# Performance work log

Hardware: AMD Instinct MI355X
Metric: run time of the kernel (lower is better)

The kernel has to match this reference:

```python
import jax, jax.numpy as jnp
import numpy as np

D_MODEL = 1024
D_FF = 4096
NUM_EXPERTS = 8
TOP_K = 2


def setup_inputs() -> dict:
    key = jax.random.key(0)
    ks = jax.random.split(key, 9)
    s = 0.02
    x = jax.random.normal(ks[0], (2, 2048, D_MODEL), dtype=jnp.float32)
    Wg = jax.random.normal(ks[1], (D_MODEL, NUM_EXPERTS), dtype=jnp.float32) * s
    bg = jnp.zeros((NUM_EXPERTS,), dtype=jnp.float32)
    W1 = jax.random.normal(ks[2], (NUM_EXPERTS, D_MODEL, D_FF), dtype=jnp.float32) * s
    b1 = jnp.zeros((NUM_EXPERTS, D_FF), dtype=jnp.float32)
    W3 = jax.random.normal(ks[3], (NUM_EXPERTS, D_MODEL, D_FF), dtype=jnp.float32) * s
    b3 = jnp.zeros((NUM_EXPERTS, D_FF), dtype=jnp.float32)
    W2 = jax.random.normal(ks[4], (NUM_EXPERTS, D_FF, D_MODEL), dtype=jnp.float32) * s
    b2 = jnp.zeros((NUM_EXPERTS, D_MODEL), dtype=jnp.float32)
    return {"x": x, "Wg": Wg, "bg": bg, "W1": W1, "b1": b1,
            "W3": W3, "b3": b3, "W2": W2, "b2": b2}


def reference(x, Wg, bg, W1, b1, W3, b3, W2, b2):
    # Gate (eval mode: no gaussian noise, no dropout)
    logits = x @ Wg + bg                                  # [b, s, E]
    probs = jax.nn.softmax(logits, axis=-1)
    top_v, top_i = jax.lax.top_k(probs, TOP_K)            # [b, s, K]
    top_v = top_v / (top_v.sum(axis=-1, keepdims=True) + 1e-6)
    # combine[b,s,e] = sum_k top_v[b,s,k] * 1[top_i[b,s,k]==e]
    onehot = jax.nn.one_hot(top_i, NUM_EXPERTS, dtype=x.dtype)  # [b, s, K, E]
    combine = jnp.einsum('bsk,bske->bse', top_v, onehot)        # [b, s, E]

    out = jnp.zeros_like(x)
    for e in range(NUM_EXPERTS):
        # SwiGLU expert FFN applied densely; masked-out tokens zeroed by combine weight
        h = jax.nn.silu(x @ W1[e] + b1[e]) * (x @ W3[e] + b3[e])   # [b, s, d_ff]
        out = out + combine[..., e:e + 1] * (h @ W2[e] + b2[e])
    return out
```

## Files before the change

kernel.cpp:

```cpp
#include <hip/hip_runtime.h>
#include <stdint.h>

#define D_MODEL 1024
#define D_FF    4096
#define NE      8
#define T_TOK   4096
#define R_TOT   8192

typedef float f32x4 __attribute__((ext_vector_type(4)));
typedef __bf16 bf16x8 __attribute__((ext_vector_type(8)));
typedef unsigned short ushort_t;

__device__ __forceinline__ ushort_t f2bf(float f) {
    unsigned int u = __float_as_uint(f);
    u += 0x7FFFu + ((u >> 16) & 1u);
    return (ushort_t)(u >> 16);
}

__device__ __forceinline__ void async16(const void* g, const void* l) {
    __builtin_amdgcn_global_load_lds(
        (const __attribute__((address_space(1))) unsigned int*)(uintptr_t)g,
        (__attribute__((address_space(3))) unsigned int*)(uintptr_t)l,
        16, 0, 0);
}

__global__ __launch_bounds__(256) void k_gate(
    const float* __restrict__ x, const float* __restrict__ Wg, const float* __restrict__ bg,
    int* __restrict__ topi, float* __restrict__ topw, int* __restrict__ counts)
{
    int wave = threadIdx.x >> 6, lane = threadIdx.x & 63;
    int t = blockIdx.x * 4 + wave;
    const float* xr = x + (size_t)t * D_MODEL;
    float acc[NE];
#pragma unroll
    for (int e = 0; e < NE; ++e) acc[e] = 0.f;
#pragma unroll
    for (int i = 0; i < D_MODEL / 64; ++i) {
        int k = i * 64 + lane;
        float xv = xr[k];
        const float4* wgp = (const float4*)(Wg + (size_t)k * NE);
        float4 w0 = wgp[0], w1 = wgp[1];
        acc[0] += xv * w0.x; acc[1] += xv * w0.y; acc[2] += xv * w0.z; acc[3] += xv * w0.w;
        acc[4] += xv * w1.x; acc[5] += xv * w1.y; acc[6] += xv * w1.z; acc[7] += xv * w1.w;
    }
#pragma unroll
    for (int off = 32; off >= 1; off >>= 1)
#pragma unroll
        for (int e = 0; e < NE; ++e) acc[e] += __shfl_down(acc[e], off, 64);
    if (lane == 0) {
        float l[NE], m = -1e30f;
#pragma unroll
        for (int e = 0; e < NE; ++e) { l[e] = acc[e] + bg[e]; m = fmaxf(m, l[e]); }
        float p[NE], Z = 0.f;
#pragma unroll
        for (int e = 0; e < NE; ++e) { p[e] = __expf(l[e] - m); Z += p[e]; }
        float invZ = 1.f / Z;
        int i0 = 0; float v0 = -1.f;
#pragma unroll
        for (int e = 0; e < NE; ++e) { p[e] *= invZ; if (p[e] > v0) { v0 = p[e]; i0 = e; } }
        int i1 = 0; float v1 = -1.f;
#pragma unroll
        for (int e = 0; e < NE; ++e) { if (e != i0 && p[e] > v1) { v1 = p[e]; i1 = e; } }
        float denom = 1.f / (v0 + v1 + 1e-6f);
        topi[t * 2 + 0] = i0; topi[t * 2 + 1] = i1;
        topw[t * 2 + 0] = v0 * denom; topw[t * 2 + 1] = v1 * denom;
        atomicAdd(&counts[i0], 1); atomicAdd(&counts[i1], 1);
    }
}

__global__ void k_scan(const int* __restrict__ counts, int* __restrict__ offsets,
                       int* __restrict__ cursors)
{
    if (threadIdx.x == 0) {
        int acc = 0;
        for (int e = 0; e < NE; ++e) { offsets[e] = acc; cursors[e] = acc; acc += counts[e]; }
    }
}

__global__ __launch_bounds__(256) void k_scatter(
    const int* __restrict__ topi_in, const float* __restrict__ topw,
    int* __restrict__ cursors, int* __restrict__ btok, float* __restrict__ bw)
{
    int t = blockIdx.x * 256 + threadIdx.x;
    int* topi = (int*)topi_in;
#pragma unroll
    for (int k = 0; k < 2; ++k) {
        int e = topi[t * 2 + k];
        int p = atomicAdd(&cursors[e], 1);
        btok[p] = t;
        bw[p] = topw[t * 2 + k];
        topi[t * 2 + k] = p;
    }
}

__global__ __launch_bounds__(256) void k_gather(
    const float* __restrict__ x, const int* __restrict__ btok, ushort_t* __restrict__ Xg)
{
    int i = blockIdx.x;
    int t = btok[i];
    float4 v = ((const float4*)(x + (size_t)t * D_MODEL))[threadIdx.x];
    ushort4 o;
    o.x = f2bf(v.x); o.y = f2bf(v.y); o.z = f2bf(v.z); o.w = f2bf(v.w);
    ((ushort4*)(Xg + (size_t)i * D_MODEL))[threadIdx.x] = o;
}

__global__ __launch_bounds__(256) void k_transpose(
    const float* __restrict__ W, ushort_t* __restrict__ Wt, int K, int N)
{
    __shared__ ushort_t tile[64 * 76];
    int e = blockIdx.z;
    const float* We = W + (size_t)e * K * N;
    ushort_t* Wte = Wt + (size_t)e * K * N;
    int nb = blockIdx.x * 64, kb = blockIdx.y * 64;
    int tn4 = (threadIdx.x & 15) * 4;
    int tk = threadIdx.x >> 4;
#pragma unroll
    for (int r = 0; r < 4; ++r) {
        int k = r * 16 + tk;
        float4 v = *(const float4*)(We + (size_t)(kb + k) * N + nb + tn4);
        tile[(tn4 + 0) * 76 + k] = f2bf(v.x);
        tile[(tn4 + 1) * 76 + k] = f2bf(v.y);
        tile[(tn4 + 2) * 76 + k] = f2bf(v.z);
        tile[(tn4 + 3) * 76 + k] = f2bf(v.w);
    }
    __syncthreads();
#pragma unroll
    for (int c = 0; c < 4; ++c) {
        int chunk = c * 256 + threadIdx.x;
        int n = chunk >> 4, kc = (chunk & 15) * 4;
        ushort4 o = *(const ushort4*)&tile[n * 76 + kc];
        *(ushort4*)(Wte + (size_t)(nb + n) * K + kb + kc) = o;
    }
}


__global__ __launch_bounds__(256, 2) void k_gemm1(
    const ushort_t* __restrict__ Xg, const ushort_t* __restrict__ W1t,
    const ushort_t* __restrict__ W3t,
    const float* __restrict__ b1, const float* __restrict__ b3,
    const int* __restrict__ counts, const int* __restrict__ offsets,
    ushort_t* __restrict__ H)
{
    __shared__ __align__(16) ushort_t sA [2][128 * 32];
    __shared__ __align__(16) ushort_t sB1[2][128 * 32];
    __shared__ __align__(16) ushort_t sB3[2][128 * 32];

    int bx = blockIdx.x;
    int lx = (bx & 7) * 9 + (bx >> 3);

    int tm = lx, e = 0, cnt = 0;
    for (; e < NE; ++e) {
        cnt = counts[e];
        int nt = (cnt + 127) >> 7;
        if (tm < nt) break;
        tm -= nt;
    }
    if (e >= NE) return;
    int row0 = offsets[e] + tm * 128;
    int rows_left = cnt - tm * 128;

    int tile_n = blockIdx.y * 128;
    int tid = threadIdx.x, wave = tid >> 6, lane = tid & 63;
    int wm = (wave >> 1) * 64, wn = (wave & 1) * 64;
    int col = lane & 15, quad = lane >> 4;

    const ushort_t* W1e = W1t + (size_t)e * D_FF * D_MODEL;
    const ushort_t* W3e = W3t + (size_t)e * D_FF * D_MODEL;

    const ushort_t* gA[2]; const ushort_t* gB1[2]; const ushort_t* gB3[2];
    unsigned ldsOff[2];
#pragma unroll
    for (int s = 0; s < 2; ++s) {
        int u = wave * 2 + s;
        int q = u * 64 + lane;
        int r = q >> 2;
        int cg = ((q & 3) ^ ((r >> 1) & 3)) * 8;
        gA[s]  = Xg  + (size_t)(row0 + r) * D_MODEL + cg;
        gB1[s] = W1e + (size_t)(tile_n + r) * D_MODEL + cg;
        gB3[s] = W3e + (size_t)(tile_n + r) * D_MODEL + cg;
        ldsOff[s] = (unsigned)u * 512;
    }

    unsigned fA[4], fB[4];
#pragma unroll
    for (int i = 0; i < 4; ++i) {
        int ra = wm + i * 16 + col;
        int rb = wn + i * 16 + col;
        fA[i] = (unsigned)ra * 32 + ((quad ^ ((ra >> 1) & 3)) * 8);
        fB[i] = (unsigned)rb * 32 + ((quad ^ ((rb >> 1) & 3)) * 8);
    }

    f32x4 acc1[4][4], acc3[4][4];
#pragma unroll
    for (int i = 0; i < 4; ++i)
#pragma unroll
        for (int j = 0; j < 4; ++j) {
            acc1[i][j] = (f32x4){0.f, 0.f, 0.f, 0.f};
            acc3[i][j] = (f32x4){0.f, 0.f, 0.f, 0.f};
        }

#define STAGE1(p, k0)                                                            \
    do {                                                                         \
        _Pragma("unroll")                                                        \
        for (int s_ = 0; s_ < 2; ++s_) {                                         \
            async16(gA[s_]  + (k0), &sA [p][ldsOff[s_]]);                        \
            async16(gB1[s_] + (k0), &sB1[p][ldsOff[s_]]);                        \
            async16(gB3[s_] + (k0), &sB3[p][ldsOff[s_]]);                        \
        }                                                                        \
    } while (0)

    STAGE1(0, 0);
    for (int t = 0; t < D_MODEL / 32; ++t) {
        int p = t & 1;
        if (t < D_MODEL / 32 - 1) {
            STAGE1(p ^ 1, (t + 1) * 32);
            asm volatile("s_waitcnt vmcnt(6)" ::: "memory");
        } else {
            asm volatile("s_waitcnt vmcnt(0)" ::: "memory");
        }
        __builtin_amdgcn_s_barrier();
        asm volatile("" ::: "memory");

        bf16x8 a[4], u[4];
#pragma unroll
        for (int i = 0; i < 4; ++i) a[i] = *(const bf16x8*)(&sA[p][fA[i]]);
#pragma unroll
        for (int j = 0; j < 4; ++j) u[j] = *(const bf16x8*)(&sB1[p][fB[j]]);
        __builtin_amdgcn_s_setprio(1);
#pragma unroll
        for (int i = 0; i < 4; ++i)
#pragma unroll
            for (int j = 0; j < 4; ++j)
                acc1[i][j] = __builtin_amdgcn_mfma_f32_16x16x32_bf16(a[i], u[j], acc1[i][j], 0, 0, 0);
        __builtin_amdgcn_s_setprio(0);
#pragma unroll
        for (int j = 0; j < 4; ++j) u[j] = *(const bf16x8*)(&sB3[p][fB[j]]);
        __builtin_amdgcn_s_setprio(1);
#pragma unroll
        for (int i = 0; i < 4; ++i)
#pragma unroll
            for (int j = 0; j < 4; ++j)
                acc3[i][j] = __builtin_amdgcn_mfma_f32_16x16x32_bf16(a[i], u[j], acc3[i][j], 0, 0, 0);
        __builtin_amdgcn_s_setprio(0);
        asm volatile("" ::: "memory");
        __builtin_amdgcn_s_barrier();
        asm volatile("" ::: "memory");
    }
#undef STAGE1

#pragma unroll
    for (int j = 0; j < 4; ++j) {
        int n = tile_n + wn + j * 16 + col;
        float bias1 = b1[e * D_FF + n];
        float bias3 = b3[e * D_FF + n];
#pragma unroll
        for (int i = 0; i < 4; ++i) {
            int rbase = wm + i * 16 + quad * 4;
#pragma unroll
            for (int r = 0; r < 4; ++r) {
                int row = rbase + r;
                if (row < rows_left) {
                    float h1 = acc1[i][j][r] + bias1;
                    float h3 = acc3[i][j][r] + bias3;
                    float s = h1 / (1.f + __expf(-h1));
                    H[(size_t)(row0 + row) * D_FF + n] = f2bf(s * h3);
                }
            }
        }
    }
}

__global__ __launch_bounds__(256, 4) void k_gemm2(
    const ushort_t* __restrict__ H, const ushort_t* __restrict__ W2t,
    const float* __restrict__ b2,
    const int* __restrict__ counts, const int* __restrict__ offsets,
    float* __restrict__ Y)
{
    __shared__ __align__(16) ushort_t sA[2][128 * 32];
    __shared__ __align__(16) ushort_t sB[2][128 * 32];

    int bx = blockIdx.x;
    int lx = (bx & 7) * 9 + (bx >> 3);

    int tm = lx, e = 0, cnt = 0;
    for (; e < NE; ++e) {
        cnt = counts[e];
        int nt = (cnt + 127) >> 7;
        if (tm < nt) break;
        tm -= nt;
    }
    if (e >= NE) return;
    int row0 = offsets[e] + tm * 128;
    int rows_left = cnt - tm * 128;

    int tile_n = blockIdx.y * 128;
    int tid = threadIdx.x, wave = tid >> 6, lane = tid & 63;
    int wm = (wave >> 1) * 64, wn = (wave & 1) * 64;
    int col = lane & 15, quad = lane >> 4;

    const ushort_t* W2e = W2t + (size_t)e * D_MODEL * D_FF;

    const ushort_t* gA[2]; const ushort_t* gB[2];
    unsigned ldsOff[2];
#pragma unroll
    for (int s = 0; s < 2; ++s) {
        int u = wave * 2 + s;
        int q = u * 64 + lane;
        int r = q >> 2;
        int cg = ((q & 3) ^ ((r >> 1) & 3)) * 8;
        gA[s] = H   + (size_t)(row0 + r) * D_FF + cg;
        gB[s] = W2e + (size_t)(tile_n + r) * D_FF + cg;
        ldsOff[s] = (unsigned)u * 512;
    }

    unsigned fA[4], fB[4];
#pragma unroll
    for (int i = 0; i < 4; ++i) {
        int ra = wm + i * 16 + col;
        int rb = wn + i * 16 + col;
        fA[i] = (unsigned)ra * 32 + ((quad ^ ((ra >> 1) & 3)) * 8);
        fB[i] = (unsigned)rb * 32 + ((quad ^ ((rb >> 1) & 3)) * 8);
    }

    f32x4 acc[4][4];
#pragma unroll
    for (int i = 0; i < 4; ++i)
#pragma unroll
        for (int j = 0; j < 4; ++j) acc[i][j] = (f32x4){0.f, 0.f, 0.f, 0.f};

#define STAGE2(p, k0)                                                            \
    do {                                                                         \
        _Pragma("unroll")                                                        \
        for (int s_ = 0; s_ < 2; ++s_) {                                         \
            async16(gA[s_] + (k0), &sA[p][ldsOff[s_]]);                          \
            async16(gB[s_] + (k0), &sB[p][ldsOff[s_]]);                          \
        }                                                                        \
    } while (0)

    STAGE2(0, 0);
    for (int t = 0; t < D_FF / 32; ++t) {
        int p = t & 1;
        if (t < D_FF / 32 - 1) {
            STAGE2(p ^ 1, (t + 1) * 32);
            asm volatile("s_waitcnt vmcnt(4)" ::: "memory");
        } else {
            asm volatile("s_waitcnt vmcnt(0)" ::: "memory");
        }
        __builtin_amdgcn_s_barrier();
        asm volatile("" ::: "memory");

        bf16x8 a[4], b[4];
#pragma unroll
        for (int i = 0; i < 4; ++i) a[i] = *(const bf16x8*)(&sA[p][fA[i]]);
#pragma unroll
        for (int j = 0; j < 4; ++j) b[j] = *(const bf16x8*)(&sB[p][fB[j]]);
        __builtin_amdgcn_s_setprio(1);
#pragma unroll
        for (int i = 0; i < 4; ++i)
#pragma unroll
            for (int j = 0; j < 4; ++j)
                acc[i][j] = __builtin_amdgcn_mfma_f32_16x16x32_bf16(a[i], b[j], acc[i][j], 0, 0, 0);
        __builtin_amdgcn_s_setprio(0);
        asm volatile("" ::: "memory");
        __builtin_amdgcn_s_barrier();
        asm volatile("" ::: "memory");
    }
#undef STAGE2

    float bias[4];
#pragma unroll
    for (int j = 0; j < 4; ++j) bias[j] = b2[e * D_MODEL + tile_n + wn + j * 16 + col];

#pragma unroll
    for (int i = 0; i < 4; ++i) {
        int rbase = wm + i * 16 + quad * 4;
#pragma unroll
        for (int r = 0; r < 4; ++r) {
            int row = rbase + r;
            if (row < rows_left) {
                float* yrow = Y + (size_t)(row0 + row) * D_MODEL + tile_n + wn + col;
#pragma unroll
                for (int j = 0; j < 4; ++j)
                    yrow[j * 16] = acc[i][j][r] + bias[j];
            }
        }
    }
}

__global__ __launch_bounds__(256) void k_combine(
    const float* __restrict__ Y, const int* __restrict__ pos,
    const float* __restrict__ topw, float* __restrict__ out)
{
    int t = blockIdx.x, c = threadIdx.x;
    int p0 = pos[t * 2 + 0], p1 = pos[t * 2 + 1];
    float w0 = topw[t * 2 + 0], w1 = topw[t * 2 + 1];
    float4 y0 = ((const float4*)(Y + (size_t)p0 * D_MODEL))[c];
    float4 y1 = ((const float4*)(Y + (size_t)p1 * D_MODEL))[c];
    float4 o;
    o.x = w0 * y0.x + w1 * y1.x;
    o.y = w0 * y0.y + w1 * y1.y;
    o.z = w0 * y0.z + w1 * y1.z;
    o.w = w0 * y0.w + w1 * y1.w;
    ((float4*)(out + (size_t)t * D_MODEL))[c] = o;
}

extern "C" void kernel_launch(void* const* d_in, const int* in_sizes, int n_in,
                              void* d_out, int out_size, void* d_ws, size_t ws_size,
                              hipStream_t stream)
{
    const float* x  = (const float*)d_in[0];
    const float* Wg = (const float*)d_in[1];
    const float* bg = (const float*)d_in[2];
    const float* W1 = (const float*)d_in[3];
    const float* b1 = (const float*)d_in[4];
    const float* W3 = (const float*)d_in[5];
    const float* b3 = (const float*)d_in[6];
    const float* W2 = (const float*)d_in[7];
    const float* b2 = (const float*)d_in[8];
    float* out = (float*)d_out;

    char* ws = (char*)d_ws;
    int*   counts  = (int*)(ws + 0);
    int*   cursors = (int*)(ws + 32);
    int*   offsets = (int*)(ws + 64);
    int*   topi    = (int*)(ws + 256);
    float* topw    = (float*)(ws + 256 + 32768);
    int*   btok    = (int*)(ws + 256 + 65536);
    float* bw      = (float*)(ws + 256 + 98304);
    char* p = ws + 131328;
    ushort_t* Xg  = (ushort_t*)p;  p += (size_t)R_TOT * D_MODEL * 2;
    ushort_t* Hb  = (ushort_t*)p;  p += (size_t)R_TOT * D_FF * 2;
    ushort_t* W1t = (ushort_t*)p;  p += (size_t)NE * D_FF * D_MODEL * 2;
    ushort_t* W3t = (ushort_t*)p;  p += (size_t)NE * D_FF * D_MODEL * 2;
    ushort_t* W2t = (ushort_t*)p;
    float* Y = (float*)W1t;

    hipMemsetAsync(ws, 0, 64, stream);

    k_gate<<<dim3(T_TOK / 4), dim3(256), 0, stream>>>(x, Wg, bg, topi, topw, counts);
    k_scan<<<dim3(1), dim3(64), 0, stream>>>(counts, offsets, cursors);
    k_scatter<<<dim3(T_TOK / 256), dim3(256), 0, stream>>>(topi, topw, cursors, btok, bw);
    k_gather<<<dim3(R_TOT), dim3(256), 0, stream>>>(x, btok, Xg);
    k_transpose<<<dim3(D_FF / 64, D_MODEL / 64, NE), dim3(256), 0, stream>>>(W1, W1t, D_MODEL, D_FF);
    k_transpose<<<dim3(D_FF / 64, D_MODEL / 64, NE), dim3(256), 0, stream>>>(W3, W3t, D_MODEL, D_FF);
    k_transpose<<<dim3(D_MODEL / 64, D_FF / 64, NE), dim3(256), 0, stream>>>(W2, W2t, D_FF, D_MODEL);
    k_gemm1<<<dim3(72, D_FF / 128), dim3(256), 0, stream>>>(Xg, W1t, W3t, b1, b3, counts, offsets, Hb);
    k_gemm2<<<dim3(72, D_MODEL / 128), dim3(256), 0, stream>>>(Hb, W2t, b2, counts, offsets, Y);
    k_combine<<<dim3(T_TOK), dim3(256), 0, stream>>>(Y, topi, topw, out);
}
```

Before: 911.2 us.

## Enlarge grouped GEMM tiles to 256 rows with 512-thread blocks and interleaved W1/W3

The transpose step now writes W1 and W3 into one interleaved buffer, so gemm1 computes a 256x256 tile covering 128 W1 columns and the matching 128 W3 columns. The SwiGLU epilogue pairs the two halves by passing the W3 accumulators through LDS. Both GEMMs move to 512-thread blocks over 256-row tiles with a 64-wide K step split into sub-phases that overlap prefetch with MFMA. The goal is more operand reuse per LDS load and fewer tiles, at the cost of more barriers, higher register pressure from the 8x4 accumulators, and more padding waste on partial per-expert row tiles.

After: 962.4 us. +5.6%, slower.

```diff
diff --git a/kernel.cpp b/kernel.cpp
--- a/kernel.cpp
+++ b/kernel.cpp
@@ -23,6 +23,9 @@
         (__attribute__((address_space(3))) unsigned int*)(uintptr_t)l,
         16, 0, 0);
 }
+
+#define FENCE() asm volatile("" ::: "memory")
+#define BAR()   do { FENCE(); __builtin_amdgcn_s_barrier(); FENCE(); } while (0)
 
 __global__ __launch_bounds__(256) void k_gate(
     const float* __restrict__ x, const float* __restrict__ Wg, const float* __restrict__ bg,
@@ -105,13 +108,14 @@
 }
 
 __global__ __launch_bounds__(256) void k_transpose(
-    const float* __restrict__ W, ushort_t* __restrict__ Wt, int K, int N)
+    const float* __restrict__ W, ushort_t* __restrict__ Wt, int K, int N, int mode)
 {
     __shared__ ushort_t tile[64 * 76];
     int e = blockIdx.z;
     const float* We = W + (size_t)e * K * N;
-    ushort_t* Wte = Wt + (size_t)e * K * N;
+    ushort_t* Wte = Wt + (size_t)e * K * (mode ? 2 * N : N);
     int nb = blockIdx.x * 64, kb = blockIdx.y * 64;
+    int nbase = (mode == 0) ? nb : ((nb >> 7) * 256 + (mode - 1) * 128 + (nb & 64));
     int tn4 = (threadIdx.x & 15) * 4;
     int tk = threadIdx.x >> 4;
 #pragma unroll
@@ -129,231 +133,276 @@
         int chunk = c * 256 + threadIdx.x;
         int n = chunk >> 4, kc = (chunk & 15) * 4;
         ushort4 o = *(const ushort4*)&tile[n * 76 + kc];
-        *(ushort4*)(Wte + (size_t)(nb + n) * K + kb + kc) = o;
-    }
-}
-
-
-__global__ __launch_bounds__(256, 2) void k_gemm1(
-    const ushort_t* __restrict__ Xg, const ushort_t* __restrict__ W1t,
-    const ushort_t* __restrict__ W3t,
+        *(ushort4*)(Wte + (size_t)(nbase + n) * K + kb + kc) = o;
+    }
+}
+
+
+__global__ __launch_bounds__(512, 2) void k_gemm1(
+    const ushort_t* __restrict__ Xg, const ushort_t* __restrict__ W13t,
     const float* __restrict__ b1, const float* __restrict__ b3,
     const int* __restrict__ counts, const int* __restrict__ offsets,
     ushort_t* __restrict__ H)
 {
-    __shared__ __align__(16) ushort_t sA [2][128 * 32];
-    __shared__ __align__(16) ushort_t sB1[2][128 * 32];
-    __shared__ __align__(16) ushort_t sB3[2][128 * 32];
+    __shared__ __align__(16) ushort_t smem[65536];
 
     int bx = blockIdx.x;
-    int lx = (bx & 7) * 9 + (bx >> 3);
+    int lx = (bx & 7) * 5 + (bx >> 3);
 
     int tm = lx, e = 0, cnt = 0;
     for (; e < NE; ++e) {
         cnt = counts[e];
-        int nt = (cnt + 127) >> 7;
+        int nt = (cnt + 255) >> 8;
         if (tm < nt) break;
         tm -= nt;
     }
     if (e >= NE) return;
-    int row0 = offsets[e] + tm * 128;
-    int rows_left = cnt - tm * 128;
+    int row0 = offsets[e] + tm * 256;
+    int rows_left = cnt - tm * 256;
+
+    int tnp = blockIdx.y * 256;
+    int tid = threadIdx.x, wave = tid >> 6, lane = tid & 63;
+    int wmp = wave >> 2, wnp = wave & 3;
+    int wm = wmp * 128, wn = wnp * 64;
+    int col = lane & 15, quad = lane >> 4;
+
+    const ushort_t* We = W13t + (size_t)e * (2 * D_FF) * D_MODEL;
+
+    const ushort_t* gA[2]; const ushort_t* gB[2]; unsigned su[2];
+#pragma unroll
+    for (int s = 0; s < 2; ++s) {
+        int q = (wave * 2 + s) * 64 + lane;
+        int r = q >> 2;
+        int c2 = (q & 3) ^ ((r >> 1) & 3);
+        gA[s] = Xg + (size_t)(row0 + r) * D_MODEL + c2 * 8;
+        gB[s] = We + (size_t)(tnp + r) * D_MODEL + c2 * 8;
+        su[s] = (unsigned)(wave * 2 + s) * 512;
+    }
+
+    int kswz = (quad ^ ((col >> 1) & 3)) * 8;
+    unsigned aoff = (unsigned)(wm + col) * 32 + kswz;
+    unsigned boff = (unsigned)(wn + col) * 32 + kswz;
+
+    f32x4 acc[8][4];
+#pragma unroll
+    for (int i = 0; i < 8; ++i)
+#pragma unroll
+        for (int j = 0; j < 4; ++j) acc[i][j] = (f32x4){0.f, 0.f, 0.f, 0.f};
+
+#define STG_A(p, h, k0) do { \
+        async16(gA[0] + (k0) + (h) * 32, &smem[(p) * 16384 + (h) * 8192 + su[0]]); \
+        async16(gA[1] + (k0) + (h) * 32, &smem[(p) * 16384 + (h) * 8192 + su[1]]); } while (0)
+#define STG_B(p, h, k0) do { \
+        async16(gB[0] + (k0) + (h) * 32, &smem[32768 + (p) * 16384 + (h) * 8192 + su[0]]); \
+        async16(gB[1] + (k0) + (h) * 32, &smem[32768 + (p) * 16384 + (h) * 8192 + su[1]]); } while (0)
+
+    STG_A(0, 0, 0); STG_B(0, 0, 0); STG_A(0, 1, 0); STG_B(0, 1, 0);
+    asm volatile("s_waitcnt vmcnt(4)" ::: "memory");
+    BAR();
+
+    const int NT = D_MODEL / 64;
+    for (int t = 0; t < NT; ++t) {
+        int p = t & 1, pn = p ^ 1;
+        int k1 = (t + 1) * 64;
+        bool pf = (t < NT - 1);
+        const ushort_t* sa0 = &smem[p * 16384];
+        const ushort_t* sb0 = &smem[32768 + p * 16384];
+        const ushort_t* sa1 = sa0 + 8192;
+        const ushort_t* sb1 = sb0 + 8192;
+        bf16x8 a[4], b[4];
+
+#pragma unroll
+        for (int i = 0; i < 4; ++i) a[i] = *(const bf16x8*)(sa0 + aoff + i * 512);
+#pragma unroll
+        for (int j = 0; j < 4; ++j) b[j] = *(const bf16x8*)(sb0 + boff + j * 512);
+        if (pf) STG_A(pn, 0, k1);
+        BAR();
+        __builtin_amdgcn_s_setprio(1);
+#pragma unroll
+        for (int i = 0; i < 4; ++i)
+#pragma unroll
+            for (int j = 0; j < 4; ++j)
+                acc[i][j] = __builtin_amdgcn_mfma_f32_16x16x32_bf16(a[i], b[j], acc[i][j], 0, 0, 0);
+        __builtin_amdgcn_s_setprio(0);
+        BAR();
+
+#pragma unroll
+        for (int i = 0; i < 4; ++i) a[i] = *(const bf16x8*)(sa0 + aoff + (i + 4) * 512);
+        if (pf) { STG_B(pn, 0, k1); asm volatile("s_waitcnt vmcnt(4)" ::: "memory"); }
+        else    {                   asm volatile("s_waitcnt vmcnt(0)" ::: "memory"); }
+        BAR();
+        __builtin_amdgcn_s_setprio(1);
+#pragma unroll
+        for (int i = 0; i < 4; ++i)
+#pragma unroll
+            for (int j = 0; j < 4; ++j)
+                acc[i + 4][j] = __builtin_amdgcn_mfma_f32_16x16x32_bf16(a[i], b[j], acc[i + 4][j], 0, 0, 0);
+        __builtin_amdgcn_s_setprio(0);
+        BAR();
+
+#pragma unroll
+        for (int i = 0; i < 4; ++i) a[i] = *(const bf16x8*)(sa1 + aoff + i * 512);
+#pragma unroll
+        for (int j = 0; j < 4; ++j) b[j] = *(const bf16x8*)(sb1 + boff + j * 512);
+        if (pf) STG_A(pn, 1, k1);
+        BAR();
+        __builtin_amdgcn_s_setprio(1);
+#pragma unroll
+        for (int i = 0; i < 4; ++i)
+#pragma unroll
+            for (int j = 0; j < 4; ++j)
+                acc[i][j] = __builtin_amdgcn_mfma_f32_16x16x32_bf16(a[i], b[j], acc[i][j], 0, 0, 0);
+        __builtin_amdgcn_s_setprio(0);
+        BAR();
+
+#pragma unroll
+        for (int i = 0; i < 4; ++i) a[i] = *(const bf16x8*)(sa1 + aoff + (i + 4) * 512);
+        if (pf) { STG_B(pn, 1, k1); asm volatile("s_waitcnt vmcnt(4)" ::: "memory"); }
+        else    {                   asm volatile("s_waitcnt vmcnt(0)" ::: "memory"); }
+        BAR();
+        __builtin_amdgcn_s_setprio(1);
+#pragma unroll
+        for (int i = 0; i < 4; ++i)
+#pragma unroll
+            for (int j = 0; j < 4; ++j)
+                acc[i + 4][j] = __builtin_amdgcn_mfma_f32_16x16x32_bf16(a[i], b[j], acc[i + 4][j], 0, 0, 0);
+        __builtin_amdgcn_s_setprio(0);
+        BAR();
+    }
+#undef STG_A
+#undef STG_B
+
+    float* eL = (float*)smem;
+    int isH3 = (wnp >= 2);
+    int pair = wmp * 2 + (wnp & 1);
+#pragma unroll
+    for (int pass = 0; pass < 2; ++pass) {
+        __syncthreads();
+        if (isH3) {
+#pragma unroll
+            for (int il = 0; il < 4; ++il) {
+                int i = pass * 4 + il;
+#pragma unroll
+                for (int j = 0; j < 4; ++j)
+#pragma unroll
+                    for (int r = 0; r < 4; ++r) {
+                        int row_l = il * 16 + quad * 4 + r;
+                        eL[(pair * 64 + row_l) * 65 + j * 16 + col] = acc[i][j][r];
+                    }
+            }
+        }
+        __syncthreads();
+        if (!isH3) {
+#pragma unroll
+            for (int il = 0; il < 4; ++il) {
+                int i = pass * 4 + il;
+                int rbase = wm + i * 16 + quad * 4;
+#pragma unroll
+                for (int j = 0; j < 4; ++j) {
+                    int n_log = blockIdx.y * 128 + (wnp & 1) * 64 + j * 16 + col;
+                    float bias1 = b1[e * D_FF + n_log];
+                    float bias3 = b3[e * D_FF + n_log];
+#pragma unroll
+                    for (int r = 0; r < 4; ++r) {
+                        int row = rbase + r;
+                        if (row < rows_left) {
+                            float h1 = acc[i][j][r] + bias1;
+                            float h3 = eL[(pair * 64 + il * 16 + quad * 4 + r) * 65 + j * 16 + col] + bias3;
+                            float s = h1 / (1.f + __expf(-h1));
+                            H[(size_t)(row0 + row) * D_FF + n_log] = f2bf(s * h3);
+                        }
+                    }
+                }
+            }
+        }
+    }
+}
+
+__global__ __launch_bounds__(512, 2) void k_gemm2(
+    const ushort_t* __restrict__ H, const ushort_t* __restrict__ W2t,
+    const float* __restrict__ b2,
+    const int* __restrict__ counts, const int* __restrict__ offsets,
+    float* __restrict__ Y)
+{
+    __shared__ __align__(16) ushort_t smem[49152];
+
+    int bx = blockIdx.x;
+    int lx = (bx & 7) * 5 + (bx >> 3);
+
+    int tm = lx, e = 0, cnt = 0;
+    for (; e < NE; ++e) {
+        cnt = counts[e];
+        int nt = (cnt + 255) >> 8;
+        if (tm < nt) break;
+        tm -= nt;
+    }
+    if (e >= NE) return;
+    int row0 = offsets[e] + tm * 256;
+    int rows_left = cnt - tm * 256;
 
     int tile_n = blockIdx.y * 128;
     int tid = threadIdx.x, wave = tid >> 6, lane = tid & 63;
     int wm = (wave >> 1) * 64, wn = (wave & 1) * 64;
     int col = lane & 15, quad = lane >> 4;
 
-    const ushort_t* W1e = W1t + (size_t)e * D_FF * D_MODEL;
-    const ushort_t* W3e = W3t + (size_t)e * D_FF * D_MODEL;
-
-    const ushort_t* gA[2]; const ushort_t* gB1[2]; const ushort_t* gB3[2];
-    unsigned ldsOff[2];
+    const ushort_t* W2e = W2t + (size_t)e * D_MODEL * D_FF;
+
+    const ushort_t* gA[2]; const ushort_t* gB; unsigned su[2], sub;
 #pragma unroll
     for (int s = 0; s < 2; ++s) {
-        int u = wave * 2 + s;
-        int q = u * 64 + lane;
+        int q = (wave * 2 + s) * 64 + lane;
         int r = q >> 2;
-        int cg = ((q & 3) ^ ((r >> 1) & 3)) * 8;
-        gA[s]  = Xg  + (size_t)(row0 + r) * D_MODEL + cg;
-        gB1[s] = W1e + (size_t)(tile_n + r) * D_MODEL + cg;
-        gB3[s] = W3e + (size_t)(tile_n + r) * D_MODEL + cg;
-        ldsOff[s] = (unsigned)u * 512;
-    }
-
-    unsigned fA[4], fB[4];
-#pragma unroll
-    for (int i = 0; i < 4; ++i) {
-        int ra = wm + i * 16 + col;
-        int rb = wn + i * 16 + col;
-        fA[i] = (unsigned)ra * 32 + ((quad ^ ((ra >> 1) & 3)) * 8);
-        fB[i] = (unsigned)rb * 32 + ((quad ^ ((rb >> 1) & 3)) * 8);
-    }
-
-    f32x4 acc1[4][4], acc3[4][4];
+        int c2 = (q & 3) ^ ((r >> 1) & 3);
+        gA[s] = H + (size_t)(row0 + r) * D_FF + c2 * 8;
+        su[s] = (unsigned)(wave * 2 + s) * 512;
+    }
+    {
+        int q = wave * 64 + lane;
+        int r = q >> 2;
+        int c2 = (q & 3) ^ ((r >> 1) & 3);
+        gB = W2e + (size_t)(tile_n + r) * D_FF + c2 * 8;
+        sub = (unsigned)wave * 512;
+    }
+
+    int kswz = (quad ^ ((col >> 1) & 3)) * 8;
+    unsigned aoff = (unsigned)(wm + col) * 32 + kswz;
+    unsigned boff = (unsigned)(wn + col) * 32 + kswz;
+
+    f32x4 acc[4][4];
 #pragma unroll
     for (int i = 0; i < 4; ++i)
 #pragma unroll
-        for (int j = 0; j < 4; ++j) {
-            acc1[i][j] = (f32x4){0.f, 0.f, 0.f, 0.f};
-            acc3[i][j] = (f32x4){0.f, 0.f, 0.f, 0.f};
-        }
-
-#define STAGE1(p, k0)                                                            \
-    do {                                                                         \
-        _Pragma("unroll")                                                        \
-        for (int s_ = 0; s_ < 2; ++s_) {                                         \
-            async16(gA[s_]  + (k0), &sA [p][ldsOff[s_]]);                        \
-            async16(gB1[s_] + (k0), &sB1[p][ldsOff[s_]]);                        \
-            async16(gB3[s_] + (k0), &sB3[p][ldsOff[s_]]);                        \
-        }                                                                        \
-    } while (0)
-
-    STAGE1(0, 0);
-    for (int t = 0; t < D_MODEL / 32; ++t) {
-        int p = t & 1;
-        if (t < D_MODEL / 32 - 1) {
-            STAGE1(p ^ 1, (t + 1) * 32);
-            asm volatile("s_waitcnt vmcnt(6)" ::: "memory");
-        } else {
-            asm volatile("s_waitcnt vmcnt(0)" ::: "memory");
-        }
-        __builtin_amdgcn_s_barrier();
-        asm volatile("" ::: "memory");
-
-        bf16x8 a[4], u[4];
-#pragma unroll
-        for (int i = 0; i < 4; ++i) a[i] = *(const bf16x8*)(&sA[p][fA[i]]);
-#pragma unroll
-        for (int j = 0; j < 4; ++j) u[j] = *(const bf16x8*)(&sB1[p][fB[j]]);
-        __builtin_amdgcn_s_setprio(1);
-#pragma unroll
-        for (int i = 0; i < 4; ++i)
-#pragma unroll
-            for (int j = 0; j < 4; ++j)
-                acc1[i][j] = __builtin_amdgcn_mfma_f32_16x16x32_bf16(a[i], u[j], acc1[i][j], 0, 0, 0);
-        __builtin_amdgcn_s_setprio(0);
-#pragma unroll
-        for (int j = 0; j < 4; ++j) u[j] = *(const bf16x8*)(&sB3[p][fB[j]]);
-        __builtin_amdgcn_s_setprio(1);
-#pragma unroll
-        for (int i = 0; i < 4; ++i)
-#pragma unroll
-            for (int j = 0; j < 4; ++j)
-                acc3[i][j] = __builtin_amdgcn_mfma_f32_16x16x32_bf16(a[i], u[j], acc3[i][j], 0, 0, 0);
-        __builtin_amdgcn_s_setprio(0);
-        asm volatile("" ::: "memory");
-        __builtin_amdgcn_s_barrier();
-        asm volatile("" ::: "memory");
-    }
-#undef STAGE1
-
-#pragma unroll
-    for (int j = 0; j < 4; ++j) {
-        int n = tile_n + wn + j * 16 + col;
-        float bias1 = b1[e * D_FF + n];
-        float bias3 = b3[e * D_FF + n];
-#pragma unroll
-        for (int i = 0; i < 4; ++i) {
-            int rbase = wm + i * 16 + quad * 4;
-#pragma unroll
-            for (int r = 0; r < 4; ++r) {
-                int row = rbase + r;
-                if (row < rows_left) {
-                    float h1 = acc1[i][j][r] + bias1;
-                    float h3 = acc3[i][j][r] + bias3;
-                    float s = h1 / (1.f + __expf(-h1));
-                    H[(size_t)(row0 + row) * D_FF + n] = f2bf(s * h3);
-                }
-            }
-        }
-    }
-}
-
-__global__ __launch_bounds__(256, 4) void k_gemm2(
-    const ushort_t* __restrict__ H, const ushort_t* __restrict__ W2t,
-    const float* __restrict__ b2,
-    const int* __restrict__ counts, const int* __restrict__ offsets,
-    float* __restrict__ Y)
-{
-    __shared__ __align__(16) ushort_t sA[2][128 * 32];
-    __shared__ __align__(16) ushort_t sB[2][128 * 32];
-
-    int bx = blockIdx.x;
-    int lx = (bx & 7) * 9 + (bx >> 3);
-
-    int tm = lx, e = 0, cnt = 0;
-    for (; e < NE; ++e) {
-        cnt = counts[e];
-        int nt = (cnt + 127) >> 7;
-        if (tm < nt) break;
-        tm -= nt;
-    }
-    if (e >= NE) return;
-    int row0 = offsets[e] + tm * 128;
-    int rows_left = cnt - tm * 128;
-
-    int tile_n = blockIdx.y * 128;
-    int tid = threadIdx.x, wave = tid >> 6, lane = tid & 63;
-    int wm = (wave >> 1) * 64, wn = (wave & 1) * 64;
-    int col = lane & 15, quad = lane >> 4;
-
-    const ushort_t* W2e = W2t + (size_t)e * D_MODEL * D_FF;
-
-    const ushort_t* gA[2]; const ushort_t* gB[2];
-    unsigned ldsOff[2];
-#pragma unroll
-    for (int s = 0; s < 2; ++s) {
-        int u = wave * 2 + s;
-        int q = u * 64 + lane;
-        int r = q >> 2;
-        int cg = ((q & 3) ^ ((r >> 1) & 3)) * 8;
-        gA[s] = H   + (size_t)(row0 + r) * D_FF + cg;
-        gB[s] = W2e + (size_t)(tile_n + r) * D_FF + cg;
-        ldsOff[s] = (unsigned)u * 512;
-    }
-
-    unsigned fA[4], fB[4];
-#pragma unroll
-    for (int i = 0; i < 4; ++i) {
-        int ra = wm + i * 16 + col;
-        int rb = wn + i * 16 + col;
-        fA[i] = (unsigned)ra * 32 + ((quad ^ ((ra >> 1) & 3)) * 8);
-        fB[i] = (unsigned)rb * 32 + ((quad ^ ((rb >> 1) & 3)) * 8);
-    }
-
-    f32x4 acc[4][4];
-#pragma unroll
-    for (int i = 0; i < 4; ++i)
-#pragma unroll
         for (int j = 0; j < 4; ++j) acc[i][j] = (f32x4){0.f, 0.f, 0.f, 0.f};
 
-#define STAGE2(p, k0)                                                            \
-    do {                                                                         \
-        _Pragma("unroll")                                                        \
-        for (int s_ = 0; s_ < 2; ++s_) {                                         \
-            async16(gA[s_] + (k0), &sA[p][ldsOff[s_]]);                          \
-            async16(gB[s_] + (k0), &sB[p][ldsOff[s_]]);                          \
-        }                                                                        \
-    } while (0)
-
-    STAGE2(0, 0);
-    for (int t = 0; t < D_FF / 32; ++t) {
-        int p = t & 1;
-        if (t < D_FF / 32 - 1) {
-            STAGE2(p ^ 1, (t + 1) * 32);
-            asm volatile("s_waitcnt vmcnt(4)" ::: "memory");
-        } else {
-            asm volatile("s_waitcnt vmcnt(0)" ::: "memory");
-        }
-        __builtin_amdgcn_s_barrier();
-        asm volatile("" ::: "memory");
-
+#define STG2_A(p, h, k0) do { \
+        async16(gA[0] + (k0) + (h) * 32, &smem[(p) * 16384 + (h) * 8192 + su[0]]); \
+        async16(gA[1] + (k0) + (h) * 32, &smem[(p) * 16384 + (h) * 8192 + su[1]]); } while (0)
+#define STG2_B(p, h, k0) \
+        async16(gB + (k0) + (h) * 32, &smem[32768 + (p) * 8192 + (h) * 4096 + sub])
+
+    STG2_A(0, 0, 0); STG2_B(0, 0, 0); STG2_A(0, 1, 0); STG2_B(0, 1, 0);
+    asm volatile("s_waitcnt vmcnt(3)" ::: "memory");
+    BAR();
+
+    const int NT = D_FF / 64;
+    for (int t = 0; t < NT; ++t) {
+        int p = t & 1, pn = p ^ 1;
+        int k1 = (t + 1) * 64;
+        bool pf = (t < NT - 1);
+        const ushort_t* sa0 = &smem[p * 16384];
+        const ushort_t* sb0 = &smem[32768 + p * 8192];
+        const ushort_t* sa1 = sa0 + 8192;
+        const ushort_t* sb1 = sb0 + 4096;
         bf16x8 a[4], b[4];
-#pragma unroll
-        for (int i = 0; i < 4; ++i) a[i] = *(const bf16x8*)(&sA[p][fA[i]]);
-#pragma unroll
-        for (int j = 0; j < 4; ++j) b[j] = *(const bf16x8*)(&sB[p][fB[j]]);
+
+#pragma unroll
+        for (int i = 0; i < 4; ++i) a[i] = *(const bf16x8*)(sa0 + aoff + i * 512);
+#pragma unroll
+        for (int j = 0; j < 4; ++j) b[j] = *(const bf16x8*)(sb0 + boff + j * 512);
+        if (pf) { STG2_A(pn, 0, k1); STG2_B(pn, 0, k1);
+                  asm volatile("s_waitcnt vmcnt(3)" ::: "memory"); }
+        else    { asm volatile("s_waitcnt vmcnt(0)" ::: "memory"); }
+        BAR();
         __builtin_amdgcn_s_setprio(1);
 #pragma unroll
         for (int i = 0; i < 4; ++i)
@@ -361,11 +410,27 @@
             for (int j = 0; j < 4; ++j)
                 acc[i][j] = __builtin_amdgcn_mfma_f32_16x16x32_bf16(a[i], b[j], acc[i][j], 0, 0, 0);
         __builtin_amdgcn_s_setprio(0);
-        asm volatile("" ::: "memory");
-        __builtin_amdgcn_s_barrier();
-        asm volatile("" ::: "memory");
-    }
-#undef STAGE2
+        BAR();
+
+#pragma unroll
+        for (int i = 0; i < 4; ++i) a[i] = *(const bf16x8*)(sa1 + aoff + i * 512);
+#pragma unroll
+        for (int j = 0; j < 4; ++j) b[j] = *(const bf16x8*)(sb1 + boff + j * 512);
+        if (pf) { STG2_A(pn, 1, k1); STG2_B(pn, 1, k1);
+                  asm volatile("s_waitcnt vmcnt(3)" ::: "memory"); }
+        else    { asm volatile("s_waitcnt vmcnt(0)" ::: "memory"); }
+        BAR();
+        __builtin_amdgcn_s_setprio(1);
+#pragma unroll
+        for (int i = 0; i < 4; ++i)
+#pragma unroll
+            for (int j = 0; j < 4; ++j)
+                acc[i][j] = __builtin_amdgcn_mfma_f32_16x16x32_bf16(a[i], b[j], acc[i][j], 0, 0, 0);
+        __builtin_amdgcn_s_setprio(0);
+        BAR();
+    }
+#undef STG2_A
+#undef STG2_B
 
     float bias[4];
 #pragma unroll
@@ -428,12 +493,11 @@
     int*   btok    = (int*)(ws + 256 + 65536);
     float* bw      = (float*)(ws + 256 + 98304);
     char* p = ws + 131328;
-    ushort_t* Xg  = (ushort_t*)p;  p += (size_t)R_TOT * D_MODEL * 2;
-    ushort_t* Hb  = (ushort_t*)p;  p += (size_t)R_TOT * D_FF * 2;
-    ushort_t* W1t = (ushort_t*)p;  p += (size_t)NE * D_FF * D_MODEL * 2;
-    ushort_t* W3t = (ushort_t*)p;  p += (size_t)NE * D_FF * D_MODEL * 2;
-    ushort_t* W2t = (ushort_t*)p;
-    float* Y = (float*)W1t;
+    ushort_t* Xg   = (ushort_t*)p;  p += (size_t)R_TOT * D_MODEL * 2;
+    ushort_t* Hb   = (ushort_t*)p;  p += (size_t)R_TOT * D_FF * 2;
+    ushort_t* W13t = (ushort_t*)p;  p += (size_t)NE * 2 * D_FF * D_MODEL * 2;
+    ushort_t* W2t  = (ushort_t*)p;
+    float* Y = (float*)W13t;
 
     hipMemsetAsync(ws, 0, 64, stream);
 
@@ -441,10 +505,10 @@
     k_scan<<<dim3(1), dim3(64), 0, stream>>>(counts, offsets, cursors);
     k_scatter<<<dim3(T_TOK / 256), dim3(256), 0, stream>>>(topi, topw, cursors, btok, bw);
     k_gather<<<dim3(R_TOT), dim3(256), 0, stream>>>(x, btok, Xg);
-    k_transpose<<<dim3(D_FF / 64, D_MODEL / 64, NE), dim3(256), 0, stream>>>(W1, W1t, D_MODEL, D_FF);
-    k_transpose<<<dim3(D_FF / 64, D_MODEL / 64, NE), dim3(256), 0, stream>>>(W3, W3t, D_MODEL, D_FF);
-    k_transpose<<<dim3(D_MODEL / 64, D_FF / 64, NE), dim3(256), 0, stream>>>(W2, W2t, D_FF, D_MODEL);
-    k_gemm1<<<dim3(72, D_FF / 128), dim3(256), 0, stream>>>(Xg, W1t, W3t, b1, b3, counts, offsets, Hb);
-    k_gemm2<<<dim3(72, D_MODEL / 128), dim3(256), 0, stream>>>(Hb, W2t, b2, counts, offsets, Y);
+    k_transpose<<<dim3(D_FF / 64, D_MODEL / 64, NE), dim3(256), 0, stream>>>(W1, W13t, D_MODEL, D_FF, 1);
+    k_transpose<<<dim3(D_FF / 64, D_MODEL / 64, NE), dim3(256), 0, stream>>>(W3, W13t, D_MODEL, D_FF, 2);
+    k_transpose<<<dim3(D_MODEL / 64, D_FF / 64, NE), dim3(256), 0, stream>>>(W2, W2t, D_FF, D_MODEL, 0);
+    k_gemm1<<<dim3(40, (2 * D_FF) / 256), dim3(512), 0, stream>>>(Xg, W13t, b1, b3, counts, offsets, Hb);
+    k_gemm2<<<dim3(40, D_MODEL / 128), dim3(512), 0, stream>>>(Hb, W2t, b2, counts, offsets, Y);
     k_combine<<<dim3(T_TOK), dim3(256), 0, stream>>>(Y, topi, topw, out);
 }
```
